# Kernel optimization log

Measured on AMD Instinct MI355X. Metric: run time of the kernel, lower is better.

## Reference

```python
import jax, jax.numpy as jnp
import numpy as np

B, C, L = 8, 1024, 1024
H = 16
D = C // H  # 64 samples per head
GROUPS = 32  # GroupNorm32: channels > 64 -> 32 groups
EPS = 1e-5


def setup_inputs() -> dict:
    key = jax.random.key(0)
    ks = jax.random.split(key, 5)
    x = jax.random.normal(ks[0], (B, C, L), dtype=jnp.float32)
    gn_weight = jnp.ones((C,), jnp.float32)
    gn_bias = jnp.zeros((C,), jnp.float32)
    qkv_w = jax.random.normal(ks[1], (3 * C, C), jnp.float32) * 0.02
    qkv_b = jax.random.normal(ks[2], (3 * C,), jnp.float32) * 0.02
    out_w = jax.random.normal(ks[3], (C, C), jnp.float32) * 0.02
    out_b = jax.random.normal(ks[4], (C,), jnp.float32) * 0.02
    return {"x": x, "gn_weight": gn_weight, "gn_bias": gn_bias,
            "qkv_w": qkv_w, "qkv_b": qkv_b, "out_w": out_w, "out_b": out_b,
            "qk_bias": 0}


def _group_norm(x, w, b):
    # x: [B, C, L]; normalize over (C//GROUPS, L) per group, in float32
    xg = x.astype(jnp.float32).reshape(B, GROUPS, -1)
    mu = xg.mean(axis=-1, keepdims=True)
    var = xg.var(axis=-1, keepdims=True)
    xn = ((xg - mu) * jax.lax.rsqrt(var + EPS)).reshape(B, C, L)
    return (xn * w[None, :, None] + b[None, :, None]).astype(x.dtype)


def reference(x, gn_weight, gn_bias, qkv_w, qkv_b, out_w, out_b, qk_bias):
    scale = 1.0 / np.sqrt(D).astype(np.float32)
    xn = _group_norm(x, gn_weight, gn_bias)
    # 1x1 conv == pointwise matmul over channels
    qkv = jnp.einsum('oc,bcl->bol', qkv_w, xn) + qkv_b[None, :, None]  # [B,3C,L]
    # reshape (B, H, 3D, L) and split exactly as torch .split(D, dim=2)
    qkv = qkv.reshape(B, H, 3 * D, L)
    q, k, v = qkv[:, :, :D], qkv[:, :, D:2 * D], qkv[:, :, 2 * D:]
    q = jnp.swapaxes(q, -1, -2) * scale  # [B,H,L,D]
    k = k * scale                        # [B,H,D,L]
    v = jnp.swapaxes(v, -1, -2)          # [B,H,L,D]
    score = jnp.einsum('bhld,bhdm->bhlm', q, k) + qk_bias  # [B,H,L,L]
    weights = jax.nn.softmax(score.astype(jnp.float32), axis=-1)
    ctx = jnp.einsum('bhlm,bhmd->bhld', weights, v)  # [B,H,L,D]
    ctx = jnp.swapaxes(ctx, -1, -2).reshape(B, C, L)
    h = jnp.einsum('oc,bcl->bol', out_w, ctx) + out_b[None, :, None]
    return xn + h  # residual uses the normalized x, as in the source
```

## Files before the change

kernel.cpp:

```cpp
#include <hip/hip_runtime.h>

using bf16x8 = __attribute__((ext_vector_type(8))) __bf16;
using f32x4  = __attribute__((ext_vector_type(4))) float;
typedef __attribute__((ext_vector_type(2))) unsigned u32x2;
typedef __attribute__((ext_vector_type(4))) unsigned u32x4;

#define DEV __device__ __forceinline__

DEV unsigned short f2bf(float f){
  unsigned u = __builtin_bit_cast(unsigned, f);
  u += 0x7fffu + ((u >> 16) & 1u);
  return (unsigned short)(u >> 16);
}

DEV void load_lds16(const void* g, void* l){
  __builtin_amdgcn_global_load_lds((const __attribute__((address_space(1))) unsigned*)g,
                                   (__attribute__((address_space(3))) unsigned*)l, 16, 0, 0);
}

DEV f32x4 mfma16(bf16x8 a, bf16x8 b, f32x4 c){
  return __builtin_amdgcn_mfma_f32_16x16x32_bf16(a, b, c, 0, 0, 0);
}

DEV float exp2_hw(float x){
  float r;
  asm("v_exp_f32 %0, %1" : "=v"(r) : "v"(x));
  return r;
}

DEV unsigned cvtpk_bf16(float a, float b){
  unsigned r;
  asm("v_cvt_pk_bf16_f32 %0, %1, %2" : "=v"(r) : "v"(a), "v"(b));
  return r;
}

DEV u32x2 tr_read(const void* p){
  u32x2 r;
  asm volatile("ds_read_b64_tr_b16 %0, %1"
               : "=v"(r)
               : "v"((const __attribute__((address_space(3))) char*)p)
               : "memory");
  return r;
}

__global__ void wconv_k(const float* __restrict__ a, unsigned short* __restrict__ o, int n4){
  for (int i = blockIdx.x * blockDim.x + threadIdx.x; i < n4; i += gridDim.x * blockDim.x){
    float4 v = reinterpret_cast<const float4*>(a)[i];
    ushort4 u;
    u.x = f2bf(v.x); u.y = f2bf(v.y); u.z = f2bf(v.z); u.w = f2bf(v.w);
    reinterpret_cast<ushort4*>(o)[i] = u;
  }
}

__global__ __launch_bounds__(256) void gn_stats_k(const float* __restrict__ x, float* __restrict__ st){
  int bg = blockIdx.x;
  const float4* xp = reinterpret_cast<const float4*>(x + (size_t)bg * 32768);
  float s = 0.f, ss = 0.f;
  for (int i = threadIdx.x; i < 8192; i += 256){
    float4 v = xp[i];
    s  += (v.x + v.y) + (v.z + v.w);
    ss += (v.x*v.x + v.y*v.y) + (v.z*v.z + v.w*v.w);
  }
  #pragma unroll
  for (int off = 32; off; off >>= 1){ s += __shfl_down(s, off); ss += __shfl_down(ss, off); }
  __shared__ float rs[4], rss[4];
  if ((threadIdx.x & 63) == 0){ rs[threadIdx.x >> 6] = s; rss[threadIdx.x >> 6] = ss; }
  __syncthreads();
  if (threadIdx.x == 0){
    s  = (rs[0] + rs[1]) + (rs[2] + rs[3]);
    ss = (rss[0] + rss[1]) + (rss[2] + rss[3]);
    float mu  = s * (1.0f / 32768.0f);
    float var = ss * (1.0f / 32768.0f) - mu * mu;
    st[bg*2]   = mu;
    st[bg*2+1] = rsqrtf(var + 1e-5f);
  }
}

__global__ __launch_bounds__(256) void gn_norm_k(const float* __restrict__ x,
                                                 const float* __restrict__ gw,
                                                 const float* __restrict__ gb,
                                                 const float* __restrict__ st,
                                                 float* __restrict__ xn,
                                                 unsigned short* __restrict__ xnt){
  int t = blockIdx.x;
  int tile = t & 15; int g = (t >> 4) & 31; int bb = t >> 9;
  float mu = st[(bb*32+g)*2], rstd = st[(bb*32+g)*2+1];
  __shared__ unsigned short lt[64*32];
  int tid = threadIdx.x;
  int l = tid & 63;
  int c0 = tid >> 6;
  size_t base = ((size_t)bb*1024 + g*32) * 1024 + tile*64;
  #pragma unroll
  for (int cb = 0; cb < 8; ++cb){
    int c = cb*4 + c0;
    size_t idx = base + (size_t)c*1024 + l;
    float xv = x[idx];
    int cg = g*32 + c;
    float v = (xv - mu) * rstd * gw[cg] + gb[cg];
    xn[idx] = v;
    lt[l*32 + c] = f2bf(v);
  }
  __syncthreads();
  int lr = tid >> 2, sl = tid & 3;
  uint4 u = *reinterpret_cast<uint4*>(&lt[lr*32 + sl*8]);
  size_t ob = ((size_t)bb*1024 + tile*64 + lr) * 1024 + g*32 + sl*8;
  *reinterpret_cast<uint4*>(&xnt[ob]) = u;
}

template<int MODE>
__global__ __launch_bounds__(256) void gemm_k(const unsigned short* __restrict__ A,
                                              const unsigned short* __restrict__ Bm,
                                              const float* __restrict__ bias,
                                              float* __restrict__ outf,
                                              unsigned short* __restrict__ qo,
                                              unsigned short* __restrict__ ko,
                                              unsigned short* __restrict__ vo){
  constexpr int MT = MODE ? 8 : 24;
  constexpr int CHUNK = MT * 8;
  __shared__ char sA[16384];
  __shared__ char sB[16384];
  const int tid = threadIdx.x;
  const int w = tid >> 6, ln = tid & 63, hi = ln >> 4, lo = ln & 15;
  const int wrow = w >> 1, wcol = w & 1;
  const int bxo = (int)blockIdx.x;
  const int bx = (bxo & 7) * CHUNK + (bxo >> 3);
  const int b = bx / (MT*8);
  const int rem = bx % (MT*8);
  const int mt = rem >> 3, nt = rem & 7;
  const char* Ag = (const char*)A + (size_t)mt*128*2048;
  const char* Bg = (const char*)Bm + ((size_t)b*1024 + nt*128)*2048;
  f32x4 acc[4][4] = {};
  for (int kk = 0; kk < 16; ++kk){
    #pragma unroll
    for (int i = 0; i < 4; ++i){
      int s = tid*16 + i*4096;
      int row = s >> 7;
      int byte = (s & 127) ^ ((row & 7) << 4);
      size_t off = (size_t)row*2048 + kk*128 + byte;
      load_lds16(Ag + off, sA + s);
      load_lds16(Bg + off, sB + s);
    }
    __syncthreads();
    #pragma unroll
    for (int ks = 0; ks < 2; ++ks){
      bf16x8 af[4], bq[4];
      #pragma unroll
      for (int mi = 0; mi < 4; ++mi){
        int row = wrow*64 + mi*16 + lo;
        af[mi] = *reinterpret_cast<const bf16x8*>(sA + row*128 + ((ks*64 + hi*16) ^ ((row & 7) << 4)));
      }
      #pragma unroll
      for (int ni = 0; ni < 4; ++ni){
        int row = wcol*64 + ni*16 + lo;
        bq[ni] = *reinterpret_cast<const bf16x8*>(sB + row*128 + ((ks*64 + hi*16) ^ ((row & 7) << 4)));
      }
      #pragma unroll
      for (int mi = 0; mi < 4; ++mi)
        #pragma unroll
        for (int ni = 0; ni < 4; ++ni)
          acc[mi][ni] = mfma16(af[mi], bq[ni], acc[mi][ni]);
    }
    __syncthreads();
  }
  if (MODE == 0){
    #pragma unroll
    for (int mi = 0; mi < 4; ++mi){
      const int o0 = mt*128 + wrow*64 + mi*16 + hi*4;
      const int hh = o0 / 192;
      const int rr = o0 % 192;
      const size_t hb = (size_t)b*16 + hh;
      float bv0 = bias[o0], bv1 = bias[o0+1], bv2 = bias[o0+2], bv3 = bias[o0+3];
      #pragma unroll
      for (int ni = 0; ni < 4; ++ni){
        const int l = nt*128 + wcol*64 + ni*16 + lo;
        if (rr < 64){
          ushort4 u;
          u.x = f2bf(acc[mi][ni][0] + bv0); u.y = f2bf(acc[mi][ni][1] + bv1);
          u.z = f2bf(acc[mi][ni][2] + bv2); u.w = f2bf(acc[mi][ni][3] + bv3);
          *reinterpret_cast<ushort4*>(qo + (hb*1024 + l)*64 + rr) = u;
        } else if (rr < 128){
          ushort4 u;
          u.x = f2bf(acc[mi][ni][0] + bv0); u.y = f2bf(acc[mi][ni][1] + bv1);
          u.z = f2bf(acc[mi][ni][2] + bv2); u.w = f2bf(acc[mi][ni][3] + bv3);
          *reinterpret_cast<ushort4*>(ko + (hb*1024 + l)*64 + (rr - 64)) = u;
        } else {
          const int d = rr - 128;
          vo[(hb*64 + d + 0)*1024 + l] = f2bf(acc[mi][ni][0] + bv0);
          vo[(hb*64 + d + 1)*1024 + l] = f2bf(acc[mi][ni][1] + bv1);
          vo[(hb*64 + d + 2)*1024 + l] = f2bf(acc[mi][ni][2] + bv2);
          vo[(hb*64 + d + 3)*1024 + l] = f2bf(acc[mi][ni][3] + bv3);
        }
      }
    }
  } else {
    #pragma unroll
    for (int mi = 0; mi < 4; ++mi){
      const int o0 = mt*128 + wrow*64 + mi*16 + hi*4;
      #pragma unroll
      for (int ni = 0; ni < 4; ++ni){
        const int l = nt*128 + wcol*64 + ni*16 + lo;
        #pragma unroll
        for (int r = 0; r < 4; ++r){
          size_t idx = ((size_t)b*1024 + o0 + r) * 1024 + l;
          outf[idx] += acc[mi][ni][r] + bias[o0 + r];
        }
      }
    }
  }
}

__global__ __launch_bounds__(256) void attn_k(const unsigned short* __restrict__ qt,
                                              const unsigned short* __restrict__ kt,
                                              const unsigned short* __restrict__ vt,
                                              unsigned short* __restrict__ ctx){
  __shared__ char sK[2][8192];
  __shared__ char sV[2][8192];
  __shared__ char sP[8192];
  const int tid = threadIdx.x;
  const int w = tid >> 6, ln = tid & 63, hi = ln >> 4, lo = ln & 15;
  const int bxo = (int)blockIdx.x;
  const int bx = (bxo & 7) * 256 + (bxo >> 3);
  const int qb = bx & 15;
  const int bh = bx >> 4;
  const int qrow = qb*64 + w*16 + lo;
  const unsigned short* qp = qt + ((size_t)bh*1024 + qrow) * 64;
  bf16x8 qf0 = *reinterpret_cast<const bf16x8*>(qp + hi*8);
  bf16x8 qf1 = *reinterpret_cast<const bf16x8*>(qp + 32 + hi*8);
  const char* kg = (const char*)(kt + (size_t)bh*65536);
  const char* vg = (const char*)(vt + (size_t)bh*65536);
  f32x4 oa[4] = {};
  float mrow[4] = {-1e30f, -1e30f, -1e30f, -1e30f};
  float lrow[4] = {0.f, 0.f, 0.f, 0.f};
  char* pw = sP + w*2048;

  auto STAGE = [&](int buf, int kb){
    #pragma unroll
    for (int i = 0; i < 2; ++i){
      int s = tid*16 + i*4096;
      int row = s >> 7;
      int byte = (s & 127) ^ ((row & 7) << 4);
      load_lds16(kg + (size_t)(kb*64 + row)*128 + byte, sK[buf] + s);
      load_lds16(vg + (size_t)row*2048 + kb*128 + byte, sV[buf] + s);
    }
  };

  const float sc2 = 0.015625f * 1.44269504f;

  STAGE(0, 0);
  asm volatile("s_waitcnt vmcnt(0)" ::: "memory");
  __builtin_amdgcn_s_barrier();

  for (int kb = 0; kb < 16; ++kb){
    const int cur = kb & 1;
    STAGE(cur ^ 1, (kb + 1) & 15);

    f32x4 sf[4];
    #pragma unroll
    for (int nf = 0; nf < 4; ++nf){
      int kr = nf*16 + lo;
      const char* kbase = sK[cur] + kr*128;
      int sw = (kr & 7) << 4;
      bf16x8 k0 = *reinterpret_cast<const bf16x8*>(kbase + ((hi*16) ^ sw));
      bf16x8 k1 = *reinterpret_cast<const bf16x8*>(kbase + ((64 + hi*16) ^ sw));
      f32x4 t = {};
      t = mfma16(qf0, k0, t);
      t = mfma16(qf1, k1, t);
      sf[nf] = t;
    }

    float m2b[4];
    #pragma unroll
    for (int r = 0; r < 4; ++r){
      float bm = fmaxf(fmaxf(sf[0][r], sf[1][r]), fmaxf(sf[2][r], sf[3][r]));
      #pragma unroll
      for (int off = 1; off < 16; off <<= 1) bm = fmaxf(bm, __shfl_xor(bm, off));
      m2b[r] = bm * sc2;
    }

    int need = (m2b[0] > mrow[0] + 8.f) | (m2b[1] > mrow[1] + 8.f) |
               (m2b[2] > mrow[2] + 8.f) | (m2b[3] > mrow[3] + 8.f);
    if (__any(need)){
      #pragma unroll
      for (int r = 0; r < 4; ++r){
        float nm = fmaxf(mrow[r], m2b[r]);
        float corr = exp2_hw(mrow[r] - nm);
        mrow[r] = nm;
        lrow[r] *= corr;
        oa[0][r] *= corr; oa[1][r] *= corr; oa[2][r] *= corr; oa[3][r] *= corr;
      }
    }

    f32x4 psum = {};
    #pragma unroll
    for (int nf = 0; nf < 4; ++nf){
      float p0 = exp2_hw(fmaf(sf[nf][0], sc2, -mrow[0]));
      float p1 = exp2_hw(fmaf(sf[nf][1], sc2, -mrow[1]));
      float p2 = exp2_hw(fmaf(sf[nf][2], sc2, -mrow[2]));
      float p3 = exp2_hw(fmaf(sf[nf][3], sc2, -mrow[3]));
      psum[0] += p0; psum[1] += p1; psum[2] += p2; psum[3] += p3;
      u32x2 pk;
      pk.x = cvtpk_bf16(p0, p1);
      pk.y = cvtpk_bf16(p2, p3);
      *reinterpret_cast<u32x2*>(pw + (nf*16 + lo)*32 + hi*8) = pk;
    }
    #pragma unroll
    for (int r = 0; r < 4; ++r){
      float ps = psum[r];
      #pragma unroll
      for (int off = 1; off < 16; off <<= 1) ps += __shfl_xor(ps, off);
      lrow[r] += ps;
    }

    asm volatile("s_waitcnt lgkmcnt(0)" ::: "memory");
    const char* pb = pw + lo*2 + hi*256;
    u32x2 t00 = tr_read(pb);
    u32x2 t01 = tr_read(pb + 128);
    u32x2 t10 = tr_read(pb + 1024);
    u32x2 t11 = tr_read(pb + 1024 + 128);
    asm volatile("s_waitcnt lgkmcnt(0)" ::: "memory");
    __builtin_amdgcn_sched_barrier(0);
    u32x4 pc0; pc0.x = t00.x; pc0.y = t00.y; pc0.z = t01.x; pc0.w = t01.y;
    u32x4 pc1; pc1.x = t10.x; pc1.y = t10.y; pc1.z = t11.x; pc1.w = t11.y;
    bf16x8 pa0 = __builtin_bit_cast(bf16x8, pc0);
    bf16x8 pa1 = __builtin_bit_cast(bf16x8, pc1);
    #pragma unroll
    for (int df = 0; df < 4; ++df){
      int vr = df*16 + lo;
      const char* vb = sV[cur] + vr*128;
      int sw = (vr & 7) << 4;
      bf16x8 v0 = *reinterpret_cast<const bf16x8*>(vb + ((hi*16) ^ sw));
      bf16x8 v1 = *reinterpret_cast<const bf16x8*>(vb + ((64 + hi*16) ^ sw));
      oa[df] = mfma16(pa0, v0, oa[df]);
      oa[df] = mfma16(pa1, v1, oa[df]);
    }

    asm volatile("s_waitcnt vmcnt(0)" ::: "memory");
    __builtin_amdgcn_s_barrier();
  }

  const int b = bh >> 4, h = bh & 15;
  float inv[4];
  #pragma unroll
  for (int r = 0; r < 4; ++r) inv[r] = __builtin_amdgcn_rcpf(lrow[r]);
  #pragma unroll
  for (int df = 0; df < 4; ++df){
    #pragma unroll
    for (int r = 0; r < 4; ++r){
      int l = qb*64 + w*16 + hi*4 + r;
      int c = h*64 + df*16 + lo;
      ctx[((size_t)b*1024 + l)*1024 + c] = f2bf(oa[df][r] * inv[r]);
    }
  }
}

extern "C" void kernel_launch(void* const* d_in, const int* in_sizes, int n_in,
                              void* d_out, int out_size, void* d_ws, size_t ws_size,
                              hipStream_t stream) {
  (void)in_sizes; (void)n_in; (void)out_size; (void)ws_size;
  const float* x     = (const float*)d_in[0];
  const float* gn_w  = (const float*)d_in[1];
  const float* gn_b  = (const float*)d_in[2];
  const float* qkv_w = (const float*)d_in[3];
  const float* qkv_b = (const float*)d_in[4];
  const float* out_w = (const float*)d_in[5];
  const float* out_b = (const float*)d_in[6];
  float* out = (float*)d_out;
  char* ws = (char*)d_ws;
  unsigned short* xnt  = (unsigned short*)(ws);
  unsigned short* qwb  = (unsigned short*)(ws + 16777216);
  unsigned short* owb  = (unsigned short*)(ws + 23068672);
  unsigned short* qt   = (unsigned short*)(ws + 25165824);
  unsigned short* kt   = (unsigned short*)(ws + 41943040);
  unsigned short* vs   = (unsigned short*)(ws + 58720256);
  unsigned short* ctxt = (unsigned short*)(ws + 75497472);
  float*          st   = (float*)(ws + 92274688);

  wconv_k<<<512, 256, 0, stream>>>(qkv_w, qwb, 786432);
  wconv_k<<<512, 256, 0, stream>>>(out_w, owb, 262144);
  gn_stats_k<<<256, 256, 0, stream>>>(x, st);
  gn_norm_k<<<4096, 256, 0, stream>>>(x, gn_w, gn_b, st, out, xnt);
  gemm_k<0><<<1536, 256, 0, stream>>>(qwb, xnt, qkv_b, nullptr, qt, kt, vs);
  attn_k<<<2048, 256, 0, stream>>>(qt, kt, vs, ctxt);
  gemm_k<1><<<512, 256, 0, stream>>>(owb, ctxt, out_b, out, nullptr, nullptr, nullptr);
}
```

Measured before the change: 335.1 us.

## Rewrite attention with 32x32 MFMA and register-resident P via permlane swaps

```diff
diff --git a/kernel.cpp b/kernel.cpp
--- a/kernel.cpp
+++ b/kernel.cpp
@@ -2,6 +2,7 @@
 
 using bf16x8 = __attribute__((ext_vector_type(8))) __bf16;
 using f32x4  = __attribute__((ext_vector_type(4))) float;
+using f32x16 = __attribute__((ext_vector_type(16))) float;
 typedef __attribute__((ext_vector_type(2))) unsigned u32x2;
 typedef __attribute__((ext_vector_type(4))) unsigned u32x4;
 
@@ -22,6 +23,10 @@
   return __builtin_amdgcn_mfma_f32_16x16x32_bf16(a, b, c, 0, 0, 0);
 }
 
+DEV f32x16 mfma32(bf16x8 a, bf16x8 b, f32x16 c){
+  return __builtin_amdgcn_mfma_f32_32x32x16_bf16(a, b, c, 0, 0, 0);
+}
+
 DEV float exp2_hw(float x){
   float r;
   asm("v_exp_f32 %0, %1" : "=v"(r) : "v"(x));
@@ -34,13 +39,8 @@
   return r;
 }
 
-DEV u32x2 tr_read(const void* p){
-  u32x2 r;
-  asm volatile("ds_read_b64_tr_b16 %0, %1"
-               : "=v"(r)
-               : "v"((const __attribute__((address_space(3))) char*)p)
-               : "memory");
-  return r;
+DEV void permswap(unsigned &a, unsigned &b){
+  asm volatile("v_permlane32_swap_b32 %0, %1" : "+v"(a), "+v"(b));
 }
 
 __global__ void wconv_k(const float* __restrict__ a, unsigned short* __restrict__ o, int n4){
@@ -215,23 +215,23 @@
                                               unsigned short* __restrict__ ctx){
   __shared__ char sK[2][8192];
   __shared__ char sV[2][8192];
-  __shared__ char sP[8192];
+  __shared__ float sRed[4][32];
   const int tid = threadIdx.x;
-  const int w = tid >> 6, ln = tid & 63, hi = ln >> 4, lo = ln & 15;
+  const int w = tid >> 6, ln = tid & 63;
+  const int hi5 = ln >> 5, lo5 = ln & 31;
   const int bxo = (int)blockIdx.x;
-  const int bx = (bxo & 7) * 256 + (bxo >> 3);
-  const int qb = bx & 15;
-  const int bh = bx >> 4;
-  const int qrow = qb*64 + w*16 + lo;
-  const unsigned short* qp = qt + ((size_t)bh*1024 + qrow) * 64;
-  bf16x8 qf0 = *reinterpret_cast<const bf16x8*>(qp + hi*8);
-  bf16x8 qf1 = *reinterpret_cast<const bf16x8*>(qp + 32 + hi*8);
+  const int bx = (bxo & 7) * 128 + (bxo >> 3);
+  const int qb = bx & 7;
+  const int bh = bx >> 3;
+  const unsigned short* qp = qt + ((size_t)bh*1024 + qb*128 + w*32 + lo5) * 64;
+  bf16x8 qreg[4];
+  #pragma unroll
+  for (int d = 0; d < 4; ++d)
+    qreg[d] = *reinterpret_cast<const bf16x8*>(qp + d*16 + hi5*8);
   const char* kg = (const char*)(kt + (size_t)bh*65536);
   const char* vg = (const char*)(vt + (size_t)bh*65536);
-  f32x4 oa[4] = {};
-  float mrow[4] = {-1e30f, -1e30f, -1e30f, -1e30f};
-  float lrow[4] = {0.f, 0.f, 0.f, 0.f};
-  char* pw = sP + w*2048;
+  f32x16 oa0 = {}, oa1 = {};
+  float m = 0.f, l = 0.f;
 
   auto STAGE = [&](int buf, int kb){
     #pragma unroll
@@ -254,102 +254,104 @@
     const int cur = kb & 1;
     STAGE(cur ^ 1, (kb + 1) & 15);
 
-    f32x4 sf[4];
-    #pragma unroll
-    for (int nf = 0; nf < 4; ++nf){
-      int kr = nf*16 + lo;
-      const char* kbase = sK[cur] + kr*128;
-      int sw = (kr & 7) << 4;
-      bf16x8 k0 = *reinterpret_cast<const bf16x8*>(kbase + ((hi*16) ^ sw));
-      bf16x8 k1 = *reinterpret_cast<const bf16x8*>(kbase + ((64 + hi*16) ^ sw));
-      f32x4 t = {};
-      t = mfma16(qf0, k0, t);
-      t = mfma16(qf1, k1, t);
-      sf[nf] = t;
-    }
-
-    float m2b[4];
-    #pragma unroll
-    for (int r = 0; r < 4; ++r){
-      float bm = fmaxf(fmaxf(sf[0][r], sf[1][r]), fmaxf(sf[2][r], sf[3][r]));
-      #pragma unroll
-      for (int off = 1; off < 16; off <<= 1) bm = fmaxf(bm, __shfl_xor(bm, off));
-      m2b[r] = bm * sc2;
-    }
-
-    int need = (m2b[0] > mrow[0] + 8.f) | (m2b[1] > mrow[1] + 8.f) |
-               (m2b[2] > mrow[2] + 8.f) | (m2b[3] > mrow[3] + 8.f);
-    if (__any(need)){
-      #pragma unroll
-      for (int r = 0; r < 4; ++r){
-        float nm = fmaxf(mrow[r], m2b[r]);
-        float corr = exp2_hw(mrow[r] - nm);
-        mrow[r] = nm;
-        lrow[r] *= corr;
-        oa[0][r] *= corr; oa[1][r] *= corr; oa[2][r] *= corr; oa[3][r] *= corr;
-      }
-    }
-
-    f32x4 psum = {};
-    #pragma unroll
-    for (int nf = 0; nf < 4; ++nf){
-      float p0 = exp2_hw(fmaf(sf[nf][0], sc2, -mrow[0]));
-      float p1 = exp2_hw(fmaf(sf[nf][1], sc2, -mrow[1]));
-      float p2 = exp2_hw(fmaf(sf[nf][2], sc2, -mrow[2]));
-      float p3 = exp2_hw(fmaf(sf[nf][3], sc2, -mrow[3]));
-      psum[0] += p0; psum[1] += p1; psum[2] += p2; psum[3] += p3;
-      u32x2 pk;
-      pk.x = cvtpk_bf16(p0, p1);
-      pk.y = cvtpk_bf16(p2, p3);
-      *reinterpret_cast<u32x2*>(pw + (nf*16 + lo)*32 + hi*8) = pk;
-    }
-    #pragma unroll
-    for (int r = 0; r < 4; ++r){
-      float ps = psum[r];
-      #pragma unroll
-      for (int off = 1; off < 16; off <<= 1) ps += __shfl_xor(ps, off);
-      lrow[r] += ps;
-    }
-
-    asm volatile("s_waitcnt lgkmcnt(0)" ::: "memory");
-    const char* pb = pw + lo*2 + hi*256;
-    u32x2 t00 = tr_read(pb);
-    u32x2 t01 = tr_read(pb + 128);
-    u32x2 t10 = tr_read(pb + 1024);
-    u32x2 t11 = tr_read(pb + 1024 + 128);
-    asm volatile("s_waitcnt lgkmcnt(0)" ::: "memory");
-    __builtin_amdgcn_sched_barrier(0);
-    u32x4 pc0; pc0.x = t00.x; pc0.y = t00.y; pc0.z = t01.x; pc0.w = t01.y;
-    u32x4 pc1; pc1.x = t10.x; pc1.y = t10.y; pc1.z = t11.x; pc1.w = t11.y;
-    bf16x8 pa0 = __builtin_bit_cast(bf16x8, pc0);
-    bf16x8 pa1 = __builtin_bit_cast(bf16x8, pc1);
-    #pragma unroll
-    for (int df = 0; df < 4; ++df){
-      int vr = df*16 + lo;
-      const char* vb = sV[cur] + vr*128;
-      int sw = (vr & 7) << 4;
-      bf16x8 v0 = *reinterpret_cast<const bf16x8*>(vb + ((hi*16) ^ sw));
-      bf16x8 v1 = *reinterpret_cast<const bf16x8*>(vb + ((64 + hi*16) ^ sw));
-      oa[df] = mfma16(pa0, v0, oa[df]);
-      oa[df] = mfma16(pa1, v1, oa[df]);
+    const char* kbase0 = sK[cur] + lo5*128;
+    const char* kbase1 = sK[cur] + (32 + lo5)*128;
+    const int ksw = (lo5 & 7) << 4;
+    f32x16 s0 = {}, s1 = {};
+    #pragma unroll
+    for (int d = 0; d < 4; ++d){
+      int off = (d*32 + hi5*16) ^ ksw;
+      bf16x8 ka = *reinterpret_cast<const bf16x8*>(kbase0 + off);
+      bf16x8 kb8 = *reinterpret_cast<const bf16x8*>(kbase1 + off);
+      s0 = mfma32(ka, qreg[d], s0);
+      s1 = mfma32(kb8, qreg[d], s1);
+    }
+
+    float t[16];
+    #pragma unroll
+    for (int i = 0; i < 16; ++i) t[i] = fmaxf(s0[i], s1[i]);
+    #pragma unroll
+    for (int st = 8; st; st >>= 1)
+      #pragma unroll
+      for (int i = 0; i < st; ++i) t[i] = fmaxf(t[i], t[i+st]);
+    float mx = fmaxf(t[0], __shfl_xor(t[0], 32));
+    float m2 = mx * sc2;
+
+    if (__builtin_expect(__any(m2 > m + 8.f), 0)){
+      float nm = fmaxf(m, m2);
+      float corr = exp2_hw(m - nm);
+      m = nm; l *= corr;
+      sRed[w][lo5] = corr;
+      __builtin_amdgcn_wave_barrier();
+      #pragma unroll
+      for (int r = 0; r < 16; ++r){
+        float cc = sRed[w][(r & 3) + 8*(r >> 2) + 4*hi5];
+        oa0[r] *= cc; oa1[r] *= cc;
+      }
+      __builtin_amdgcn_wave_barrier();
+    }
+
+    float ps[16];
+    #pragma unroll
+    for (int i = 0; i < 16; ++i){
+      float p0 = exp2_hw(fmaf(s0[i], sc2, -m));
+      float p1 = exp2_hw(fmaf(s1[i], sc2, -m));
+      s0[i] = p0; s1[i] = p1;
+      ps[i] = p0 + p1;
+    }
+    #pragma unroll
+    for (int st = 8; st; st >>= 1)
+      #pragma unroll
+      for (int i = 0; i < st; ++i) ps[i] += ps[i+st];
+    l += ps[0] + __shfl_xor(ps[0], 32);
+
+    bf16x8 pa[4];
+    #pragma unroll
+    for (int sl = 0; sl < 4; ++sl){
+      const int c0 = 2*(sl & 1), c1 = c0 + 1;
+      unsigned w0, w1, w2, w3;
+      if (sl < 2){
+        w0 = cvtpk_bf16(s0[4*c0+0], s0[4*c0+1]);
+        w1 = cvtpk_bf16(s0[4*c0+2], s0[4*c0+3]);
+        w2 = cvtpk_bf16(s0[4*c1+0], s0[4*c1+1]);
+        w3 = cvtpk_bf16(s0[4*c1+2], s0[4*c1+3]);
+      } else {
+        w0 = cvtpk_bf16(s1[4*c0+0], s1[4*c0+1]);
+        w1 = cvtpk_bf16(s1[4*c0+2], s1[4*c0+3]);
+        w2 = cvtpk_bf16(s1[4*c1+0], s1[4*c1+1]);
+        w3 = cvtpk_bf16(s1[4*c1+2], s1[4*c1+3]);
+      }
+      permswap(w0, w2);
+      permswap(w1, w3);
+      u32x4 pc; pc.x = w0; pc.y = w1; pc.z = w2; pc.w = w3;
+      pa[sl] = __builtin_bit_cast(bf16x8, pc);
+    }
+
+    const char* vb0 = sV[cur] + lo5*128;
+    const char* vb1 = sV[cur] + (32 + lo5)*128;
+    #pragma unroll
+    for (int sl = 0; sl < 4; ++sl){
+      int off = (sl*32 + hi5*16) ^ ksw;
+      bf16x8 v0 = *reinterpret_cast<const bf16x8*>(vb0 + off);
+      bf16x8 v1 = *reinterpret_cast<const bf16x8*>(vb1 + off);
+      oa0 = mfma32(pa[sl], v0, oa0);
+      oa1 = mfma32(pa[sl], v1, oa1);
     }
 
     asm volatile("s_waitcnt vmcnt(0)" ::: "memory");
     __builtin_amdgcn_s_barrier();
   }
 
+  sRed[w][lo5] = l;
+  __builtin_amdgcn_wave_barrier();
   const int b = bh >> 4, h = bh & 15;
-  float inv[4];
   #pragma unroll
-  for (int r = 0; r < 4; ++r) inv[r] = __builtin_amdgcn_rcpf(lrow[r]);
-  #pragma unroll
-  for (int df = 0; df < 4; ++df){
-    #pragma unroll
-    for (int r = 0; r < 4; ++r){
-      int l = qb*64 + w*16 + hi*4 + r;
-      int c = h*64 + df*16 + lo;
-      ctx[((size_t)b*1024 + l)*1024 + c] = f2bf(oa[df][r] * inv[r]);
-    }
+  for (int r = 0; r < 16; ++r){
+    int ql = (r & 3) + 8*(r >> 2) + 4*hi5;
+    float inv = __builtin_amdgcn_rcpf(sRed[w][ql]);
+    size_t rowb = ((size_t)b*1024 + qb*128 + w*32 + ql) * 1024 + h*64;
+    ctx[rowb + lo5]      = f2bf(oa0[r] * inv);
+    ctx[rowb + 32 + lo5] = f2bf(oa1[r] * inv);
   }
 }
 
@@ -380,6 +382,6 @@
   gn_stats_k<<<256, 256, 0, stream>>>(x, st);
   gn_norm_k<<<4096, 256, 0, stream>>>(x, gn_w, gn_b, st, out, xnt);
   gemm_k<0><<<1536, 256, 0, stream>>>(qwb, xnt, qkv_b, nullptr, qt, kt, vs);
-  attn_k<<<2048, 256, 0, stream>>>(qt, kt, vs, ctxt);
+  attn_k<<<1024, 256, 0, stream>>>(qt, kt, vs, ctxt);
   gemm_k<1><<<512, 256, 0, stream>>>(owb, ctxt, out_b, out, nullptr, nullptr, nullptr);
 }
```

After: 288.1 us. 1.16x faster.
